# Performance work log

Hardware: AMD Instinct MI355X
Metric: run time of the kernel (lower is better)

Reference implementation:

```python
import jax, jax.numpy as jnp
import numpy as np
import math

DIM = 256
PATCH = 16  # Patchnum
H = W = 64  # feature_size
B = 16


def _conv(x, w, pad):
    # x: [B,C,H,W], w: [O,I,kh,kw]
    return jax.lax.conv_general_dilated(
        x, w, window_strides=(1, 1), padding=[(pad, pad), (pad, pad)],
        dimension_numbers=('NCHW', 'OIHW', 'NCHW'))


def setup_inputs() -> dict:
    key = jax.random.key(0)
    ks = jax.random.split(key, 6)
    fan = DIM * 9
    s3 = 1.0 / math.sqrt(fan)
    s1 = 1.0 / math.sqrt(DIM)
    return {
        'e': jax.random.normal(ks[0], (B, DIM, H, W), dtype=jnp.float32),
        'pam_out': jax.random.normal(ks[1], (B, DIM, PATCH, PATCH), dtype=jnp.float32),
        'q_w': jax.random.uniform(ks[2], (DIM, DIM, 3, 3), jnp.float32, -s3, s3),
        'k_w': jax.random.uniform(ks[3], (DIM, DIM, 3, 3), jnp.float32, -s3, s3),
        'v_w': jax.random.uniform(ks[4], (DIM, DIM, 3, 3), jnp.float32, -s3, s3),
        'proj_w': jax.random.uniform(ks[5], (DIM, DIM, 1, 1), jnp.float32, -s1, s1),
    }


def reference(e, pam_out, q_w, k_w, v_w, proj_w):
    b, c, h, w = e.shape
    # AdaptiveAvgPool2d((PATCH, PATCH)) with h % PATCH == 0 -> mean pooling
    fh, fw = h // PATCH, w // PATCH
    max_e = e.reshape(b, c, PATCH, fh, PATCH, fw).mean(axis=(3, 5))
    q = _conv(max_e, q_w, 1).reshape(b, c, PATCH * PATCH)      # [b,c,P^2]
    k = _conv(pam_out, k_w, 1).reshape(b, c, PATCH * PATCH)    # [b,c,P^2]
    v = _conv(e, v_w, 1).reshape(b, c, h * w)                  # [b,c,HW]
    # L2 normalize along token dim (torch F.normalize, eps=1e-12)
    q = q / jnp.maximum(jnp.linalg.norm(q, axis=-1, keepdims=True), 1e-12)
    k = k / jnp.maximum(jnp.linalg.norm(k, axis=-1, keepdims=True), 1e-12)
    attn = jnp.einsum('bcn,bdn->bcd', q, k) / math.sqrt(c)     # [b,c,c]
    attn = jax.nn.softmax(attn, axis=-1)
    out = jnp.einsum('bcd,bdn->bcn', attn, v).reshape(b, c, h, w)
    out = _conv(out, proj_w, 0) + e
    return out
```

## Files before the change

kernel.cpp:

```cpp
#include <hip/hip_runtime.h>
#include <hip/hip_bf16.h>

#define NB 16
#define NC 256
#define NPIX 4096

typedef __attribute__((ext_vector_type(8))) short short8;
typedef __attribute__((ext_vector_type(4))) short short4v;
typedef __attribute__((ext_vector_type(4))) float f32x4;

static __device__ __forceinline__ ushort f2bf(float f) {
    __hip_bfloat16 h = __float2bfloat16(f);
    return *(ushort*)&h;
}

static __device__ __forceinline__ void gload_lds16(const ushort* g, ushort* l) {
    __builtin_amdgcn_global_load_lds(
        (const __attribute__((address_space(1))) unsigned int*)g,
        (__attribute__((address_space(3))) unsigned int*)l, 16, 0, 0);
}

__global__ void __launch_bounds__(256) prep_k(
    const float* __restrict__ e, const float* __restrict__ pam,
    const float* __restrict__ qw, const float* __restrict__ kw,
    const float* __restrict__ vw, const float* __restrict__ pw,
    ushort* __restrict__ maxeT, ushort* __restrict__ pamT,
    ushort* __restrict__ wqT, ushort* __restrict__ wkT,
    ushort* __restrict__ pbf, ushort* __restrict__ vwT,
    float* __restrict__ qnorm, float* __restrict__ knorm) {
    __shared__ float smem[9216];
    int blk = blockIdx.x, t = threadIdx.x;
    if (blk < 512) {
        int isPam = blk >> 8;
        int bb = blk & 255;
        int b = bb >> 4, cg = bb & 15;
        float (*lt)[256] = (float(*)[256])smem;
        if (!isPam) {
            int py = t >> 4, px = t & 15;
#pragma unroll
            for (int cc = 0; cc < 16; ++cc) {
                int c = cg * 16 + cc;
                const float* p = e + (size_t)(b * 256 + c) * NPIX;
                float s = 0.f;
#pragma unroll
                for (int r = 0; r < 4; ++r) {
                    float4 v = *(const float4*)(p + (py * 4 + r) * 64 + px * 4);
                    s += v.x + v.y + v.z + v.w;
                }
                lt[cc][t] = s * 0.0625f;
            }
        } else {
#pragma unroll
            for (int cc = 0; cc < 16; ++cc)
                lt[cc][t] = pam[(size_t)(b * 256 + cg * 16 + cc) * 256 + t];
        }
        __syncthreads();
        ushort* dstb = (isPam ? pamT : maxeT) + (size_t)b * 65536 + (size_t)t * 256 + cg * 16;
#pragma unroll
        for (int g = 0; g < 2; ++g) {
            short8 v;
#pragma unroll
            for (int k = 0; k < 8; ++k) v[k] = (short)f2bf(lt[g * 8 + k][t]);
            *(short8*)(dstb + g * 8) = v;
        }
    } else if (blk < 1024) {
        int idx = blk - 512;
        const float* src = (idx < 256) ? qw : kw;
        ushort* dst = (idx < 256) ? wqT : wkT;
        int o = idx & 255;
        float wv[9];
#pragma unroll
        for (int j = 0; j < 9; ++j) wv[j] = src[(size_t)o * 2304 + t * 9 + j];
#pragma unroll
        for (int j = 0; j < 9; ++j) dst[(size_t)j * 65536 + (size_t)o * 256 + t] = f2bf(wv[j]);
    } else if (blk < 1040) {
        int base = (blk - 1024) * 4096;
        for (int g = 0; g < 16; ++g) {
            int idx = base + g * 256 + t;
            pbf[idx] = f2bf(pw[idx]);
        }
    } else if (blk < 1104) {
        int d0 = (blk - 1040) * 4;
        float* lt = smem;
        for (int u = 0; u < 36; ++u) lt[u * 256 + t] = vw[(size_t)d0 * 2304 + u * 256 + t];
        __syncthreads();
#pragma unroll
        for (int r = 0; r < 9; ++r) {
            int idx = r * 256 + t;
            int i = idx / 9, j = idx % 9;
            short4v v;
#pragma unroll
            for (int dd = 0; dd < 4; ++dd) v[dd] = (short)f2bf(lt[dd * 2304 + idx]);
            *(short4v*)(vwT + ((size_t)(j * 256 + i)) * 256 + d0) = v;
        }
    } else {
        for (int g = 0; g < 16; ++g) {
            qnorm[g * 256 + t] = 0.f;
            knorm[g * 256 + t] = 0.f;
        }
    }
}

__global__ void __launch_bounds__(256, 2) conv16_mfma(const ushort* __restrict__ maxeT,
                                                      const ushort* __restrict__ pamT,
                                                      const ushort* __restrict__ wqT,
                                                      const ushort* __restrict__ wkT,
                                                      ushort* __restrict__ qb,
                                                      ushort* __restrict__ kTb,
                                                      float* __restrict__ qnorm,
                                                      float* __restrict__ knorm) {
    int blk = blockIdx.x;
    int qk = blk >> 8;
    int b  = (blk >> 4) & 15;
    int og = (blk >> 2) & 3;
    int tg = blk & 3;
    const ushort* inT = qk ? pamT : maxeT;
    const ushort* wt  = qk ? wkT : wqT;
    ushort* outp      = qk ? kTb : qb;
    float* nrm        = qk ? knorm : qnorm;
    int tid = threadIdx.x, wid = tid >> 6, lane = tid & 63;
    int wm = wid >> 1, wn = wid & 1;
    int kq = lane >> 4, l16 = lane & 15;
    int ty0 = tg * 4;
    __shared__ ushort Bs[96][256];
    __shared__ ushort As[2][64][64];
    const ushort* itb = inT + (size_t)b * 65536;
    {
#pragma unroll
        for (int j = 0; j < 12; ++j) {
            int d = (j * 4 + wid) * 64 + lane;
            int tok = d >> 5, u = d & 31;
            int lr = tok >> 4, tx = tok & 15;
            int gy = min(max(ty0 - 1 + lr, 0), 15);
            gload_lds16(itb + (gy * 16 + tx) * 256 + ((u ^ (tok & 7)) * 8),
                        &Bs[0][0] + (size_t)(j * 4 + wid) * 512);
        }
    }
    int aoff[2];
#pragma unroll
    for (int j = 0; j < 2; ++j) {
        int d = (j * 4 + wid) * 64 + lane;
        int o = d >> 3, u = d & 7;
        aoff[j] = (og * 64 + o) * 256 + ((u ^ (o & 7)) * 8);
    }
    auto stageA = [&](int s, int buf) {
        const ushort* base = wt + (size_t)(s >> 2) * 65536 + (s & 3) * 64;
#pragma unroll
        for (int j = 0; j < 2; ++j)
            gload_lds16(base + aoff[j], &As[buf][0][0] + (size_t)(j * 4 + wid) * 512);
    };
    stageA(0, 0);
    stageA(1, 1);
    __syncthreads();
    f32x4 acc[2][2];
#pragma unroll
    for (int mf = 0; mf < 2; ++mf)
#pragma unroll
        for (int nf = 0; nf < 2; ++nf) acc[mf][nf] = (f32x4){0.f, 0.f, 0.f, 0.f};
    const short8 zf = {};
    for (int s = 0; s < 36; ++s) {
        int tap = s >> 2, kh = s & 3;
        int dy = tap / 3 - 1, dx = tap % 3 - 1;
        const ushort* bp[2]; bool ok[2]; int lt7[2];
#pragma unroll
        for (int nf = 0; nf < 2; ++nf) {
            int n = tg * 64 + wn * 32 + nf * 16 + l16;
            int ny = (n >> 4) + dy, nx = (n & 15) + dx;
            ok[nf] = ((unsigned)ny < 16u) && ((unsigned)nx < 16u);
            int lrc = min(max(ny - ty0 + 1, 0), 5);
            int nxc = min(max(nx, 0), 15);
            int ltok = lrc * 16 + nxc;
            bp[nf] = &Bs[ltok][0];
            lt7[nf] = ltok & 7;
        }
#pragma unroll
        for (int kc = 0; kc < 2; ++kc) {
            int ua = kc * 4 + kq;
            int ub = kh * 8 + kc * 4 + kq;
            short8 af[2], bfr[2];
#pragma unroll
            for (int mf = 0; mf < 2; ++mf) {
                int o = wm * 32 + mf * 16 + l16;
                af[mf] = *(const short8*)(&As[s & 1][o][(ua ^ (o & 7)) * 8]);
            }
#pragma unroll
            for (int nf = 0; nf < 2; ++nf) {
                short8 v = *(const short8*)(bp[nf] + ((ub ^ lt7[nf]) * 8));
                bfr[nf] = ok[nf] ? v : zf;
            }
#pragma unroll
            for (int mf = 0; mf < 2; ++mf)
#pragma unroll
                for (int nf = 0; nf < 2; ++nf)
                    acc[mf][nf] = __builtin_amdgcn_mfma_f32_16x16x32_bf16(af[mf], bfr[nf], acc[mf][nf], 0, 0, 0);
        }
        __syncthreads();
        if (s + 2 < 36) stageA(s + 2, s & 1);
    }
    float ss[2][4];
#pragma unroll
    for (int mf = 0; mf < 2; ++mf)
#pragma unroll
        for (int r = 0; r < 4; ++r) ss[mf][r] = 0.f;
#pragma unroll
    for (int mf = 0; mf < 2; ++mf)
#pragma unroll
        for (int nf = 0; nf < 2; ++nf)
#pragma unroll
            for (int r = 0; r < 4; ++r) ss[mf][r] += acc[mf][nf][r] * acc[mf][nf][r];
#pragma unroll
    for (int mf = 0; mf < 2; ++mf)
#pragma unroll
        for (int r = 0; r < 4; ++r) {
#pragma unroll
            for (int off = 1; off < 16; off <<= 1) ss[mf][r] += __shfl_xor(ss[mf][r], off, 64);
        }
    if (l16 == 0) {
#pragma unroll
        for (int mf = 0; mf < 2; ++mf)
#pragma unroll
            for (int r = 0; r < 4; ++r)
                atomicAdd(&nrm[b * 256 + og * 64 + wm * 32 + mf * 16 + kq * 4 + r], ss[mf][r]);
    }
    ushort* ob = outp + (size_t)b * 65536;
#pragma unroll
    for (int mf = 0; mf < 2; ++mf)
#pragma unroll
        for (int nf = 0; nf < 2; ++nf) {
            int col = tg * 64 + wn * 32 + nf * 16 + l16;
#pragma unroll
            for (int r = 0; r < 4; ++r) {
                int row = og * 64 + wm * 32 + mf * 16 + kq * 4 + r;
                ob[(size_t)row * 256 + col] = f2bf(acc[mf][nf][r]);
            }
        }
}

__global__ void __launch_bounds__(512) attn_mfma(const ushort* __restrict__ qb,
                                                 const ushort* __restrict__ kTb,
                                                 const float* __restrict__ qnorm,
                                                 const float* __restrict__ knorm,
                                                 ushort* __restrict__ attnT) {
    int blk = blockIdx.x;
    int b = (blk & 7) + 8 * ((blk >> 3) & 1);
    int cg = blk >> 4;
    int tid = threadIdx.x, wid = tid >> 6, lane = tid & 63;
    int rw = wid & 3, chf = wid >> 2;
    int kq = lane >> 4, l16 = lane & 15;
    int c0w = cg * 64 + rw * 16;
    int lrow = rw * 16 + kq * 4;
    f32x4 acc[8];
#pragma unroll
    for (int nf = 0; nf < 8; ++nf) acc[nf] = (f32x4){0.f, 0.f, 0.f, 0.f};
    const ushort* qp = qb + (size_t)b * 65536;
    const ushort* kp = kTb + (size_t)b * 65536 + (size_t)(chf * 128) * 256;
    for (int kc = 0; kc < 8; ++kc) {
        short8 af = *(const short8*)(qp + (size_t)(c0w + l16) * 256 + kc * 32 + kq * 8);
#pragma unroll
        for (int nf = 0; nf < 8; ++nf) {
            short8 bf = *(const short8*)(kp + (size_t)(nf * 16 + l16) * 256 + kc * 32 + kq * 8);
            acc[nf] = __builtin_amdgcn_mfma_f32_16x16x32_bf16(af, bf, acc[nf], 0, 0, 0);
        }
    }
    float rq[4], rk[8];
#pragma unroll
    for (int r = 0; r < 4; ++r)
        rq[r] = rsqrtf(fmaxf(qnorm[b * 256 + c0w + kq * 4 + r], 1e-24f)) * 0.0625f;
#pragma unroll
    for (int nf = 0; nf < 8; ++nf)
        rk[nf] = rsqrtf(fmaxf(knorm[b * 256 + chf * 128 + nf * 16 + l16], 1e-24f));
#pragma unroll
    for (int nf = 0; nf < 8; ++nf)
#pragma unroll
        for (int r = 0; r < 4; ++r) acc[nf][r] *= rq[r] * rk[nf];
    __shared__ float red[64][2];
    float m4[4], s4[4];
#pragma unroll
    for (int r = 0; r < 4; ++r) {
        float m = -1e30f;
#pragma unroll
        for (int nf = 0; nf < 8; ++nf) m = fmaxf(m, acc[nf][r]);
#pragma unroll
        for (int off = 1; off < 16; off <<= 1) m = fmaxf(m, __shfl_xor(m, off, 64));
        m4[r] = m;
    }
    if (l16 == 0) {
#pragma unroll
        for (int r = 0; r < 4; ++r) red[lrow + r][chf] = m4[r];
    }
    __syncthreads();
#pragma unroll
    for (int r = 0; r < 4; ++r) m4[r] = fmaxf(red[lrow + r][0], red[lrow + r][1]);
    __syncthreads();
#pragma unroll
    for (int r = 0; r < 4; ++r) {
        float s = 0.f;
#pragma unroll
        for (int nf = 0; nf < 8; ++nf) {
            float ex = __expf(acc[nf][r] - m4[r]);
            acc[nf][r] = ex;
            s += ex;
        }
#pragma unroll
        for (int off = 1; off < 16; off <<= 1) s += __shfl_xor(s, off, 64);
        s4[r] = s;
    }
    if (l16 == 0) {
#pragma unroll
        for (int r = 0; r < 4; ++r) red[lrow + r][chf] = s4[r];
    }
    __syncthreads();
#pragma unroll
    for (int r = 0; r < 4; ++r) {
        float inv = 1.0f / (red[lrow + r][0] + red[lrow + r][1]);
#pragma unroll
        for (int nf = 0; nf < 8; ++nf) acc[nf][r] *= inv;
    }
    ushort* ap = attnT + (size_t)b * 65536;
#pragma unroll
    for (int nf = 0; nf < 8; ++nf) {
        int d = chf * 128 + nf * 16 + l16;
        short4v v;
#pragma unroll
        for (int r = 0; r < 4; ++r) v[r] = (short)f2bf(acc[nf][r]);
        *(short4v*)(ap + (size_t)d * 256 + c0w + kq * 4) = v;
    }
}

__global__ void __launch_bounds__(512) mproj_mfma(const ushort* __restrict__ pbf,
                                                  const ushort* __restrict__ attnT,
                                                  ushort* __restrict__ Mbf) {
    int blk = blockIdx.x;
    int b = (blk & 7) + 8 * ((blk >> 3) & 1);
    int og = blk >> 4;
    int tid = threadIdx.x, wid = tid >> 6, lane = tid & 63;
    int rw = wid & 3, chf = wid >> 2;
    int kq = lane >> 4, l16 = lane & 15;
    int o0w = og * 64 + rw * 16;
    f32x4 acc[8];
#pragma unroll
    for (int nf = 0; nf < 8; ++nf) acc[nf] = (f32x4){0.f, 0.f, 0.f, 0.f};
    const ushort* ap = attnT + (size_t)b * 65536 + (size_t)(chf * 128) * 256;
    for (int kc = 0; kc < 8; ++kc) {
        short8 af = *(const short8*)(pbf + (size_t)(o0w + l16) * 256 + kc * 32 + kq * 8);
#pragma unroll
        for (int nf = 0; nf < 8; ++nf) {
            short8 bf = *(const short8*)(ap + (size_t)(nf * 16 + l16) * 256 + kc * 32 + kq * 8);
            acc[nf] = __builtin_amdgcn_mfma_f32_16x16x32_bf16(af, bf, acc[nf], 0, 0, 0);
        }
    }
    ushort* mb = Mbf + (size_t)b * 65536;
#pragma unroll
    for (int nf = 0; nf < 8; ++nf)
#pragma unroll
        for (int r = 0; r < 4; ++r)
            mb[(size_t)(o0w + kq * 4 + r) * 256 + chf * 128 + nf * 16 + l16] = f2bf(acc[nf][r]);
}

__global__ void __launch_bounds__(512) weff_mfma(const ushort* __restrict__ Mbf,
                                                 const ushort* __restrict__ vwT,
                                                 ushort* __restrict__ wbf) {
    int blk = blockIdx.x;
    int i = blk >> 3;
    int b = (blk & 7) + 8 * (i >> 4);
    int j = i & 15;
    if (j >= 9) return;
    int tid = threadIdx.x;
    int wid = tid >> 6, lane = tid & 63;
    int wm = wid >> 1, wn = wid & 1;
    int kq = lane >> 4, l16 = lane & 15;
    f32x4 acc[4][8];
#pragma unroll
    for (int mf = 0; mf < 4; ++mf)
#pragma unroll
        for (int nf = 0; nf < 8; ++nf) acc[mf][nf] = (f32x4){0.f, 0.f, 0.f, 0.f};
    const ushort* abase = Mbf + (size_t)b * 65536 + (size_t)(wm * 64 + l16) * 256 + kq * 8;
    const ushort* bbase = vwT + (size_t)(j * 256 + wn * 128 + l16) * 256 + kq * 8;
    for (int kc = 0; kc < 8; ++kc) {
        int d0 = kc * 32;
        short8 af[4], bfr[8];
#pragma unroll
        for (int mf = 0; mf < 4; ++mf) af[mf] = *(const short8*)(abase + mf * 16 * 256 + d0);
#pragma unroll
        for (int nf = 0; nf < 8; ++nf) bfr[nf] = *(const short8*)(bbase + nf * 16 * 256 + d0);
#pragma unroll
        for (int mf = 0; mf < 4; ++mf)
#pragma unroll
            for (int nf = 0; nf < 8; ++nf)
                acc[mf][nf] = __builtin_amdgcn_mfma_f32_16x16x32_bf16(af[mf], bfr[nf], acc[mf][nf], 0, 0, 0);
    }
    ushort* wout = wbf + ((size_t)(b * 9 + j)) * 65536;
#pragma unroll
    for (int mf = 0; mf < 4; ++mf) {
        int o = wm * 64 + mf * 16 + kq * 4;
#pragma unroll
        for (int nf = 0; nf < 8; ++nf) {
            int ic = wn * 128 + nf * 16 + l16;
#pragma unroll
            for (int r = 0; r < 4; ++r)
                wout[(size_t)(o + r) * 256 + ic] = f2bf(acc[mf][nf][r]);
        }
    }
}

__global__ void __launch_bounds__(512, 4) bigconv_mfma(const float* __restrict__ e,
                                                       const ushort* __restrict__ wbf,
                                                       float* __restrict__ out) {
    int blk = blockIdx.x;
    int ibf = blk >> 3;
    int b = (blk & 7) + 8 * (ibf >> 6);
    int rem = ibf & 63;
    int pt = rem >> 1, oh = rem & 1;
    int y0 = pt * 2;
    int tid = threadIdx.x, wid = tid >> 6, lane = tid & 63;
    int wm = wid >> 1, wn = wid & 1;
    int kq = lane >> 4, l16 = lane & 15;
    __shared__ ushort Bs[4][64][64];
    __shared__ ushort As[2][128][64];
    f32x4 acc[2][4];
#pragma unroll
    for (int mf = 0; mf < 2; ++mf)
#pragma unroll
        for (int nf = 0; nf < 4; ++nf) acc[mf][nf] = (f32x4){0.f, 0.f, 0.f, 0.f};
    const float* eb = e + (size_t)b * NC * NPIX;
    const ushort* wb = wbf + (size_t)b * 589824;
    const short8 zf = {};
    int c2 = tid & 31, rr = tid >> 5;
    int sr = rr >> 2, sq = rr & 3;
    int syc = min(max(y0 - 1 + sr, 0), 63);
    int ao[2], asd[2];
#pragma unroll
    for (int j = 0; j < 2; ++j) {
        int du = (j * 8 + wid) * 64 + lane;
        ao[j] = du >> 3;
        asd[j] = (lane & 7) ^ (ao[j] & 7);
    }

    for (int ci = 0; ci < 4; ++ci) {
        __syncthreads();
        {
            const float* s0 = eb + ((size_t)(ci * 64 + 2 * c2) * 64 + syc) * 64 + sq * 16;
            const float* s1 = s0 + NPIX;
            float4 va[4], vb[4];
#pragma unroll
            for (int q = 0; q < 4; ++q) va[q] = *(const float4*)(s0 + q * 4);
#pragma unroll
            for (int q = 0; q < 4; ++q) vb[q] = *(const float4*)(s1 + q * 4);
            uint* bsrow = (uint*)&Bs[sr][0][0];
#pragma unroll
            for (int q = 0; q < 4; ++q) {
#pragma unroll
                for (int m2 = 0; m2 < 4; ++m2) {
                    int px = sq * 16 + q * 4 + m2;
                    float f0 = ((const float*)&va[q])[m2];
                    float f1 = ((const float*)&vb[q])[m2];
                    uint pk = (uint)f2bf(f0) | ((uint)f2bf(f1) << 16);
                    int s = (c2 >> 2) ^ (px & 7);
                    bsrow[px * 32 + s * 4 + (c2 & 3)] = pk;
                }
            }
        }
        {
#pragma unroll
            for (int j = 0; j < 2; ++j) {
                const ushort* src = wb + (size_t)(oh * 128 + ao[j]) * 256 + ci * 64 + asd[j] * 8;
                gload_lds16(src, &As[0][0][0] + (size_t)(j * 8 + wid) * 512);
            }
        }
        __syncthreads();
        int cur = 0;
        for (int tap = 0; tap < 9; ++tap) {
            if (tap < 8) {
#pragma unroll
                for (int j = 0; j < 2; ++j) {
                    const ushort* src = wb + (size_t)(tap + 1) * 65536 +
                                        (size_t)(oh * 128 + ao[j]) * 256 + ci * 64 + asd[j] * 8;
                    gload_lds16(src, &As[cur ^ 1][0][0] + (size_t)(j * 8 + wid) * 512);
                }
            }
            {
                int dy = tap / 3 - 1, dx = tap % 3 - 1;
                int rl = wn + dy + 1;
                bool rowok = (unsigned)(y0 + wn + dy) < 64u;
                const ushort* bp[4]; bool ok[4]; int p7[4];
#pragma unroll
                for (int nf = 0; nf < 4; ++nf) {
                    int pxr = nf * 16 + l16 + dx;
                    ok[nf] = rowok && ((unsigned)pxr < 64u);
                    int pxc = min(max(pxr, 0), 63);
                    bp[nf] = &Bs[rl][pxc][0];
                    p7[nf] = pxc & 7;
                }
#pragma unroll
                for (int kc = 0; kc < 2; ++kc) {
                    int sd = kc * 4 + kq;
                    short8 af[2];
#pragma unroll
                    for (int mf = 0; mf < 2; ++mf) {
                        int o = wm * 32 + mf * 16 + l16;
                        af[mf] = *(const short8*)(&As[cur][o][(sd ^ (o & 7)) * 8]);
                    }
                    short8 bfr[4];
#pragma unroll
                    for (int nf = 0; nf < 4; ++nf) {
                        short8 v = *(const short8*)(bp[nf] + (sd ^ p7[nf]) * 8);
                        bfr[nf] = ok[nf] ? v : zf;
                    }
#pragma unroll
                    for (int mf = 0; mf < 2; ++mf)
#pragma unroll
                        for (int nf = 0; nf < 4; ++nf)
                            acc[mf][nf] = __builtin_amdgcn_mfma_f32_16x16x32_bf16(af[mf], bfr[nf], acc[mf][nf], 0, 0, 0);
                }
            }
            __syncthreads();
            cur ^= 1;
        }
    }
    int pcol0 = pt * 128 + wn * 64 + l16;
    float* ob = out + (size_t)b * NC * NPIX;
#pragma unroll
    for (int mf = 0; mf < 2; ++mf) {
        int o = oh * 128 + wm * 32 + mf * 16 + kq * 4;
#pragma unroll
        for (int nf = 0; nf < 4; ++nf) {
            int p = pcol0 + nf * 16;
#pragma unroll
            for (int r = 0; r < 4; ++r) {
                size_t idx = (size_t)(o + r) * NPIX + p;
                ob[idx] = acc[mf][nf][r] + eb[idx];
            }
        }
    }
}

extern "C" void kernel_launch(void* const* d_in, const int* in_sizes, int n_in,
                              void* d_out, int out_size, void* d_ws, size_t ws_size,
                              hipStream_t stream) {
    const float* e   = (const float*)d_in[0];
    const float* pam = (const float*)d_in[1];
    const float* qw  = (const float*)d_in[2];
    const float* kw  = (const float*)d_in[3];
    const float* vw  = (const float*)d_in[4];
    const float* pw  = (const float*)d_in[5];
    float* out = (float*)d_out;
    float* ws  = (float*)d_ws;

    ushort* wbf  = (ushort*)ws;
    float*  S    = ws + 4718592;
    ushort* maxeT = (ushort*)S;
    ushort* pamT  = (ushort*)(S + 524288);
    ushort* wqT   = (ushort*)(S + 1048576);
    ushort* wkT   = (ushort*)(S + 1343488);
    ushort* pbf   = (ushort*)(S + 1638400);
    ushort* vwT   = (ushort*)(S + 1671168);
    float*  qnorm = S + 1966080;
    float*  knorm = S + 1970176;
    ushort* qb    = (ushort*)ws;
    ushort* kTb   = (ushort*)(ws + 524288);
    ushort* attnT = maxeT;
    ushort* Mbf   = pamT;

    prep_k<<<1105, 256, 0, stream>>>(e, pam, qw, kw, vw, pw,
                                     maxeT, pamT, wqT, wkT, pbf, vwT, qnorm, knorm);
    conv16_mfma<<<512, 256, 0, stream>>>(maxeT, pamT, wqT, wkT, qb, kTb, qnorm, knorm);
    attn_mfma<<<64, 512, 0, stream>>>(qb, kTb, qnorm, knorm, attnT);
    mproj_mfma<<<64, 512, 0, stream>>>(pbf, attnT, Mbf);
    weff_mfma<<<256, 512, 0, stream>>>(Mbf, vwT, wbf);
    bigconv_mfma<<<1024, 512, 0, stream>>>(e, wbf, out);
}
```

Baseline: 212.6 us.

## Enlarge bigconv tile to four output rows and split mean-pool prep blocks

```diff
diff --git a/kernel.cpp b/kernel.cpp
--- a/kernel.cpp
+++ b/kernel.cpp
@@ -30,32 +30,34 @@
     float* __restrict__ qnorm, float* __restrict__ knorm) {
     __shared__ float smem[9216];
     int blk = blockIdx.x, t = threadIdx.x;
-    if (blk < 512) {
-        int isPam = blk >> 8;
-        int bb = blk & 255;
+    if (blk < 1024) {
+        int b = blk >> 6, c0 = (blk & 63) * 4;
+        int py = t >> 4, px4 = (t & 15) * 4;
+        float s[4];
+#pragma unroll
+        for (int cc = 0; cc < 4; ++cc) {
+            const float* p = e + (size_t)(b * 256 + c0 + cc) * NPIX;
+            float a = 0.f;
+#pragma unroll
+            for (int r = 0; r < 4; ++r) {
+                float4 v = *(const float4*)(p + (py * 4 + r) * 64 + px4);
+                a += v.x + v.y + v.z + v.w;
+            }
+            s[cc] = a * 0.0625f;
+        }
+        short4v v;
+#pragma unroll
+        for (int cc = 0; cc < 4; ++cc) v[cc] = (short)f2bf(s[cc]);
+        *(short4v*)(maxeT + (size_t)b * 65536 + (size_t)t * 256 + c0) = v;
+    } else if (blk < 1280) {
+        int bb = blk - 1024;
         int b = bb >> 4, cg = bb & 15;
         float (*lt)[256] = (float(*)[256])smem;
-        if (!isPam) {
-            int py = t >> 4, px = t & 15;
-#pragma unroll
-            for (int cc = 0; cc < 16; ++cc) {
-                int c = cg * 16 + cc;
-                const float* p = e + (size_t)(b * 256 + c) * NPIX;
-                float s = 0.f;
-#pragma unroll
-                for (int r = 0; r < 4; ++r) {
-                    float4 v = *(const float4*)(p + (py * 4 + r) * 64 + px * 4);
-                    s += v.x + v.y + v.z + v.w;
-                }
-                lt[cc][t] = s * 0.0625f;
-            }
-        } else {
-#pragma unroll
-            for (int cc = 0; cc < 16; ++cc)
-                lt[cc][t] = pam[(size_t)(b * 256 + cg * 16 + cc) * 256 + t];
-        }
+#pragma unroll
+        for (int cc = 0; cc < 16; ++cc)
+            lt[cc][t] = pam[(size_t)(b * 256 + cg * 16 + cc) * 256 + t];
         __syncthreads();
-        ushort* dstb = (isPam ? pamT : maxeT) + (size_t)b * 65536 + (size_t)t * 256 + cg * 16;
+        ushort* dstb = pamT + (size_t)b * 65536 + (size_t)t * 256 + cg * 16;
 #pragma unroll
         for (int g = 0; g < 2; ++g) {
             short8 v;
@@ -63,8 +65,8 @@
             for (int k = 0; k < 8; ++k) v[k] = (short)f2bf(lt[g * 8 + k][t]);
             *(short8*)(dstb + g * 8) = v;
         }
-    } else if (blk < 1024) {
-        int idx = blk - 512;
+    } else if (blk < 1792) {
+        int idx = blk - 1280;
         const float* src = (idx < 256) ? qw : kw;
         ushort* dst = (idx < 256) ? wqT : wkT;
         int o = idx & 255;
@@ -73,14 +75,14 @@
         for (int j = 0; j < 9; ++j) wv[j] = src[(size_t)o * 2304 + t * 9 + j];
 #pragma unroll
         for (int j = 0; j < 9; ++j) dst[(size_t)j * 65536 + (size_t)o * 256 + t] = f2bf(wv[j]);
-    } else if (blk < 1040) {
-        int base = (blk - 1024) * 4096;
+    } else if (blk < 1808) {
+        int base = (blk - 1792) * 4096;
         for (int g = 0; g < 16; ++g) {
             int idx = base + g * 256 + t;
             pbf[idx] = f2bf(pw[idx]);
         }
-    } else if (blk < 1104) {
-        int d0 = (blk - 1040) * 4;
+    } else if (blk < 1872) {
+        int d0 = (blk - 1808) * 4;
         float* lt = smem;
         for (int u = 0; u < 36; ++u) lt[u * 256 + t] = vw[(size_t)d0 * 2304 + u * 256 + t];
         __syncthreads();
@@ -408,25 +410,26 @@
                                                        float* __restrict__ out) {
     int blk = blockIdx.x;
     int ibf = blk >> 3;
-    int b = (blk & 7) + 8 * (ibf >> 6);
-    int rem = ibf & 63;
+    int b = (blk & 7) + 8 * (ibf >> 5);
+    int rem = ibf & 31;
     int pt = rem >> 1, oh = rem & 1;
-    int y0 = pt * 2;
+    int y0 = pt * 4;
     int tid = threadIdx.x, wid = tid >> 6, lane = tid & 63;
-    int wm = wid >> 1, wn = wid & 1;
+    int wr = wid >> 1, wo = wid & 1;
     int kq = lane >> 4, l16 = lane & 15;
-    __shared__ ushort Bs[4][64][64];
+    __shared__ ushort Bs[6][64][64];
     __shared__ ushort As[2][128][64];
-    f32x4 acc[2][4];
-#pragma unroll
-    for (int mf = 0; mf < 2; ++mf)
+    f32x4 acc[4][4];
+#pragma unroll
+    for (int mf = 0; mf < 4; ++mf)
 #pragma unroll
         for (int nf = 0; nf < 4; ++nf) acc[mf][nf] = (f32x4){0.f, 0.f, 0.f, 0.f};
     const float* eb = e + (size_t)b * NC * NPIX;
     const ushort* wb = wbf + (size_t)b * 589824;
     const short8 zf = {};
     int c2 = tid & 31, rr = tid >> 5;
-    int sr = rr >> 2, sq = rr & 3;
+    int sr = rr >> 1, sq = rr & 1;
+    bool bstage = (rr < 12);
     int syc = min(max(y0 - 1 + sr, 0), 63);
     int ao[2], asd[2];
 #pragma unroll
@@ -438,25 +441,28 @@
 
     for (int ci = 0; ci < 4; ++ci) {
         __syncthreads();
-        {
-            const float* s0 = eb + ((size_t)(ci * 64 + 2 * c2) * 64 + syc) * 64 + sq * 16;
+        if (bstage) {
+            const float* s0 = eb + ((size_t)(ci * 64 + 2 * c2) * 64 + syc) * 64 + sq * 32;
             const float* s1 = s0 + NPIX;
-            float4 va[4], vb[4];
-#pragma unroll
-            for (int q = 0; q < 4; ++q) va[q] = *(const float4*)(s0 + q * 4);
-#pragma unroll
-            for (int q = 0; q < 4; ++q) vb[q] = *(const float4*)(s1 + q * 4);
             uint* bsrow = (uint*)&Bs[sr][0][0];
 #pragma unroll
-            for (int q = 0; q < 4; ++q) {
-#pragma unroll
-                for (int m2 = 0; m2 < 4; ++m2) {
-                    int px = sq * 16 + q * 4 + m2;
-                    float f0 = ((const float*)&va[q])[m2];
-                    float f1 = ((const float*)&vb[q])[m2];
-                    uint pk = (uint)f2bf(f0) | ((uint)f2bf(f1) << 16);
-                    int s = (c2 >> 2) ^ (px & 7);
-                    bsrow[px * 32 + s * 4 + (c2 & 3)] = pk;
+            for (int h = 0; h < 2; ++h) {
+                float4 va[4], vb[4];
+#pragma unroll
+                for (int q = 0; q < 4; ++q) va[q] = *(const float4*)(s0 + h * 16 + q * 4);
+#pragma unroll
+                for (int q = 0; q < 4; ++q) vb[q] = *(const float4*)(s1 + h * 16 + q * 4);
+#pragma unroll
+                for (int q = 0; q < 4; ++q) {
+#pragma unroll
+                    for (int m2 = 0; m2 < 4; ++m2) {
+                        int px = sq * 32 + h * 16 + q * 4 + m2;
+                        float f0 = ((const float*)&va[q])[m2];
+                        float f1 = ((const float*)&vb[q])[m2];
+                        uint pk = (uint)f2bf(f0) | ((uint)f2bf(f1) << 16);
+                        int s = (c2 >> 2) ^ (px & 7);
+                        bsrow[px * 32 + s * 4 + (c2 & 3)] = pk;
+                    }
                 }
             }
         }
@@ -480,8 +486,8 @@
             }
             {
                 int dy = tap / 3 - 1, dx = tap % 3 - 1;
-                int rl = wn + dy + 1;
-                bool rowok = (unsigned)(y0 + wn + dy) < 64u;
+                int rl = wr + dy + 1;
+                bool rowok = (unsigned)(y0 + wr + dy) < 64u;
                 const ushort* bp[4]; bool ok[4]; int p7[4];
 #pragma unroll
                 for (int nf = 0; nf < 4; ++nf) {
@@ -494,10 +500,10 @@
 #pragma unroll
                 for (int kc = 0; kc < 2; ++kc) {
                     int sd = kc * 4 + kq;
-                    short8 af[2];
-#pragma unroll
-                    for (int mf = 0; mf < 2; ++mf) {
-                        int o = wm * 32 + mf * 16 + l16;
+                    short8 af[4];
+#pragma unroll
+                    for (int mf = 0; mf < 4; ++mf) {
+                        int o = wo * 64 + mf * 16 + l16;
                         af[mf] = *(const short8*)(&As[cur][o][(sd ^ (o & 7)) * 8]);
                     }
                     short8 bfr[4];
@@ -507,7 +513,7 @@
                         bfr[nf] = ok[nf] ? v : zf;
                     }
 #pragma unroll
-                    for (int mf = 0; mf < 2; ++mf)
+                    for (int mf = 0; mf < 4; ++mf)
 #pragma unroll
                         for (int nf = 0; nf < 4; ++nf)
                             acc[mf][nf] = __builtin_amdgcn_mfma_f32_16x16x32_bf16(af[mf], bfr[nf], acc[mf][nf], 0, 0, 0);
@@ -517,14 +523,14 @@
             cur ^= 1;
         }
     }
-    int pcol0 = pt * 128 + wn * 64 + l16;
+    int prow = y0 + wr;
     float* ob = out + (size_t)b * NC * NPIX;
 #pragma unroll
-    for (int mf = 0; mf < 2; ++mf) {
-        int o = oh * 128 + wm * 32 + mf * 16 + kq * 4;
+    for (int mf = 0; mf < 4; ++mf) {
+        int o = oh * 128 + wo * 64 + mf * 16 + kq * 4;
 #pragma unroll
         for (int nf = 0; nf < 4; ++nf) {
-            int p = pcol0 + nf * 16;
+            int p = prow * 64 + nf * 16 + l16;
 #pragma unroll
             for (int r = 0; r < 4; ++r) {
                 size_t idx = (size_t)(o + r) * NPIX + p;
@@ -561,11 +567,11 @@
     ushort* attnT = maxeT;
     ushort* Mbf   = pamT;
 
-    prep_k<<<1105, 256, 0, stream>>>(e, pam, qw, kw, vw, pw,
+    prep_k<<<1873, 256, 0, stream>>>(e, pam, qw, kw, vw, pw,
                                      maxeT, pamT, wqT, wkT, pbf, vwT, qnorm, knorm);
     conv16_mfma<<<512, 256, 0, stream>>>(maxeT, pamT, wqT, wkT, qb, kTb, qnorm, knorm);
     attn_mfma<<<64, 512, 0, stream>>>(qb, kTb, qnorm, knorm, attnT);
     mproj_mfma<<<64, 512, 0, stream>>>(pbf, attnT, Mbf);
     weff_mfma<<<256, 512, 0, stream>>>(Mbf, vwT, wbf);
-    bigconv_mfma<<<1024, 512, 0, stream>>>(e, wbf, out);
-}
+    bigconv_mfma<<<512, 512, 0, stream>>>(e, wbf, out);
+}
```

Measured after the change: 204.4 us. 1.04x faster.
